# Kernel optimization log

Measured on AMD Instinct MI355X. Metric: run time of the kernel, lower is better.

## Reference

```python
import jax, jax.numpy as jnp
import numpy as np

N_NODES = 50000
N_EDGES = 800000
IN_SIZE, HID_SIZE, OUT_SIZE = 512, 128, 64


def _graph_conv(feat, src, dst, W, b, out_norm, in_norm, activation=None):
    # DGL GraphConv with norm='both': h' = D_in^{-1/2} A D_out^{-1/2} (X W) + b
    x = feat * out_norm[:, None]          # scale by source (out-degree) norm
    x = x @ W                             # dense transform first (in >= out)
    msg = x[src]                          # gather per-edge messages [E, d]
    agg = jax.ops.segment_sum(msg, dst, num_segments=N_NODES)
    h = agg * in_norm[:, None] + b
    if activation is not None:
        h = activation(h)
    return h


def setup_inputs() -> dict:
    key = jax.random.key(0)
    k1, k2, k3, k4, k5, k6, k7 = jax.random.split(key, 7)
    features = jax.random.normal(k1, (N_NODES, IN_SIZE), dtype=jnp.float32)
    src = jax.random.randint(k2, (N_EDGES,), 0, N_NODES, dtype=jnp.int64)
    dst = jax.random.randint(k3, (N_EDGES,), 0, N_NODES, dtype=jnp.int64)
    # Glorot-style init as in dglnn.GraphConv
    W1 = jax.random.normal(k4, (IN_SIZE, HID_SIZE), dtype=jnp.float32) * (1.0 / np.sqrt(IN_SIZE))
    b1 = jnp.zeros((HID_SIZE,), dtype=jnp.float32)
    W2 = jax.random.normal(k5, (HID_SIZE, OUT_SIZE), dtype=jnp.float32) * (1.0 / np.sqrt(HID_SIZE))
    b2 = jnp.zeros((OUT_SIZE,), dtype=jnp.float32)
    return {"features": features, "W1": W1, "b1": b1, "W2": W2, "b2": b2,
            "src": src, "dst": dst}


def reference(features, W1, b1, W2, b2, src, dst):
    ones = jnp.ones((N_EDGES,), dtype=features.dtype)
    out_deg = jax.ops.segment_sum(ones, src, num_segments=N_NODES)
    in_deg = jax.ops.segment_sum(ones, dst, num_segments=N_NODES)
    out_norm = jax.lax.rsqrt(jnp.clip(out_deg, 1.0))  # deg clamped to >=1 as in DGL
    in_norm = jax.lax.rsqrt(jnp.clip(in_deg, 1.0))
    h = _graph_conv(features, src, dst, W1, b1, out_norm, in_norm, activation=jax.nn.relu)
    # dropout omitted (eval mode)
    h = _graph_conv(h, src, dst, W2, b2, out_norm, in_norm, activation=None)
    return h
```

## Files before the change

### kernel.cpp

```cpp
#include <hip/hip_runtime.h>

#define N_NODES 50000
#define IN_SIZE 512
#define HID 128
#define OUT 64
#define NB 256
#define SHIFT 7
#define NBUCK 391
#define NBINS8 12500

typedef _Float16 f16x8 __attribute__((ext_vector_type(8)));
typedef _Float16 f16x4 __attribute__((ext_vector_type(4)));
typedef float    f32x4 __attribute__((ext_vector_type(4)));

__device__ __forceinline__ bool detect_w(const int* p, int t, int* sh) {
    if (t < 64) {
        unsigned long long m = __ballot(p[2 * t + 1] == 0);
        if (t == 0) *sh = (m == ~0ull) ? 1 : 0;
    }
    __syncthreads();
    return *sh != 0;
}

__device__ __forceinline__ int load_idx(const void* p, int e, bool w) {
    return w ? (int)((const long long*)p)[e] : ((const int*)p)[e];
}

__global__ __launch_bounds__(256) void k_hist_wt(const void* __restrict__ srcp,
                                                 const void* __restrict__ dstp,
                                                 int* __restrict__ hist,
                                                 unsigned int* __restrict__ spart,
                                                 int E, int EPB,
                                                 const float* __restrict__ W1, _Float16* __restrict__ W1T,
                                                 const float* __restrict__ W2, _Float16* __restrict__ W2T) {
    const int t = threadIdx.x, b = blockIdx.x;
    if (b >= NB) {
        int i = (b - NB) * 256 + t;
        if (i < IN_SIZE * HID) {
            int k = i >> 7, n = i & (HID - 1);
            W1T[(size_t)n * IN_SIZE + k] = (_Float16)W1[i];
        } else {
            int j = i - IN_SIZE * HID;
            if (j < HID * OUT) {
                int k = j >> 6, n = j & (OUT - 1);
                W2T[(size_t)n * HID + k] = (_Float16)W2[j];
            }
        }
        return;
    }
    __shared__ unsigned int sbins[NBINS8];
    __shared__ int dbins[NBUCK];
    __shared__ int shw;
    for (int i = t; i < NBINS8; i += 256) sbins[i] = 0;
    for (int i = t; i < NBUCK; i += 256) dbins[i] = 0;
    bool w = detect_w((const int*)dstp, t, &shw);
    __syncthreads();
    int eend = min(E, (b + 1) * EPB);
    for (int e = b * EPB + t; e < eend; e += 256) {
        int s = load_idx(srcp, e, w);
        int d = load_idx(dstp, e, w);
        atomicAdd(&dbins[d >> SHIFT], 1);
        atomicAdd(&sbins[s >> 2], 1u << ((s & 3) << 3));
    }
    __syncthreads();
    for (int i = t; i < NBUCK; i += 256) hist[i * NB + b] = dbins[i];
    for (int i = t; i < NBINS8; i += 256) spart[(size_t)b * NBINS8 + i] = sbins[i];
}

__global__ __launch_bounds__(256) void k_scanA(int* __restrict__ hist, int* __restrict__ bsum) {
    __shared__ int s[256];
    const int t = threadIdx.x, g = blockIdx.x;
    int v = hist[g * NB + t];
    s[t] = v;
    __syncthreads();
    for (int off = 1; off < 256; off <<= 1) {
        int u = (t >= off) ? s[t - off] : 0;
        __syncthreads();
        s[t] += u;
        __syncthreads();
    }
    hist[g * NB + t] = s[t] - v;
    if (t == 255) bsum[g] = s[255];
}

__global__ __launch_bounds__(512) void k_scanB(const int* __restrict__ bsum, int* __restrict__ bb) {
    __shared__ int s[512];
    const int t = threadIdx.x;
    int v = (t < NBUCK) ? bsum[t] : 0;
    s[t] = v;
    __syncthreads();
    for (int off = 1; off < 512; off <<= 1) {
        int u = (t >= off) ? s[t - off] : 0;
        __syncthreads();
        s[t] += u;
        __syncthreads();
    }
    if (t <= NBUCK) bb[t] = s[t] - v;
}

__global__ __launch_bounds__(256) void k_cscatter(const void* __restrict__ srcp,
                                                  const void* __restrict__ dstp,
                                                  const int* __restrict__ hist,
                                                  const int* __restrict__ bb,
                                                  unsigned int* __restrict__ tmp,
                                                  int E, int EPB) {
    __shared__ int cur[NBUCK];
    __shared__ int shw;
    const int t = threadIdx.x, b = blockIdx.x;
    for (int i = t; i < NBUCK; i += 256) cur[i] = hist[i * NB + b] + bb[i];
    bool w = detect_w((const int*)dstp, t, &shw);
    __syncthreads();
    int eend = min(E, (b + 1) * EPB);
    for (int e = b * EPB + t; e < eend; e += 256) {
        int s = load_idx(srcp, e, w);
        int d = load_idx(dstp, e, w);
        int pos = atomicAdd(&cur[d >> SHIFT], 1);
        tmp[pos] = (unsigned int)s | ((unsigned int)(d & 127) << 16);
    }
}

__global__ __launch_bounds__(256) void k_fine(const unsigned int* __restrict__ tmp,
                                              const int* __restrict__ bb,
                                              const unsigned int* __restrict__ partial,
                                              int* __restrict__ rp,
                                              int* __restrict__ esrc,
                                              float* __restrict__ innorm,
                                              float* __restrict__ onorm) {
    __shared__ int fcnt[128];
    __shared__ int sc[128];
    __shared__ int fcur[128];
    __shared__ int rs[256][4];
    const int t = threadIdx.x, u = blockIdx.x;
    const int e0 = bb[u], e1 = bb[u + 1];
    if (t < 128) fcnt[t] = 0;
    __syncthreads();
    for (int e = e0 + t; e < e1; e += 256)
        atomicAdd(&fcnt[tmp[e] >> 16], 1);
    {
        const int wrd = t & 31, grp = t >> 5;
        const int wd = u * 32 + wrd;
        int c0 = 0, c1 = 0, c2 = 0, c3 = 0;
        if (wd < NBINS8) {
            for (int b = grp * 32; b < grp * 32 + 32; ++b) {
                unsigned int v = partial[(size_t)b * NBINS8 + wd];
                c0 += (int)(v & 255u);
                c1 += (int)((v >> 8) & 255u);
                c2 += (int)((v >> 16) & 255u);
                c3 += (int)(v >> 24);
            }
        }
        rs[t][0] = c0; rs[t][1] = c1; rs[t][2] = c2; rs[t][3] = c3;
    }
    __syncthreads();
    if (t < 32) {
        const int wd = u * 32 + t;
        if (wd < NBINS8) {
            int d0 = 0, d1 = 0, d2 = 0, d3 = 0;
            for (int g = 0; g < 8; ++g) {
                d0 += rs[g * 32 + t][0]; d1 += rs[g * 32 + t][1];
                d2 += rs[g * 32 + t][2]; d3 += rs[g * 32 + t][3];
            }
            if (d0 < 1) d0 = 1; if (d1 < 1) d1 = 1;
            if (d2 < 1) d2 = 1; if (d3 < 1) d3 = 1;
            int n0 = 4 * wd;
            if (n0     < N_NODES) onorm[n0]     = 1.0f / sqrtf((float)d0);
            if (n0 + 1 < N_NODES) onorm[n0 + 1] = 1.0f / sqrtf((float)d1);
            if (n0 + 2 < N_NODES) onorm[n0 + 2] = 1.0f / sqrtf((float)d2);
            if (n0 + 3 < N_NODES) onorm[n0 + 3] = 1.0f / sqrtf((float)d3);
        }
    }
    if (t < 128) sc[t] = fcnt[t];
    __syncthreads();
    for (int off = 1; off < 128; off <<= 1) {
        int v = (t < 128 && t >= off) ? sc[t - off] : 0;
        __syncthreads();
        if (t < 128) sc[t] += v;
        __syncthreads();
    }
    if (t < 128) {
        int base = e0 + sc[t] - fcnt[t];
        fcur[t] = base;
        int node = u * 128 + t;
        if (node < N_NODES) {
            rp[node] = base;
            int c = fcnt[t]; if (c < 1) c = 1;
            innorm[node] = 1.0f / sqrtf((float)c);
        }
    }
    if (u == NBUCK - 1 && t == 0) rp[N_NODES] = e1;
    __syncthreads();
    for (int e = e0 + t; e < e1; e += 256) {
        unsigned int p = tmp[e];
        int pos = atomicAdd(&fcur[p >> 16], 1);
        esrc[pos] = (int)(p & 0xFFFFu);
    }
}

#define LDA 40
__global__ __launch_bounds__(256) void k_gemm1_mfma(const float* __restrict__ A,
                                                    const _Float16* __restrict__ BT,
                                                    const float* __restrict__ onorm,
                                                    _Float16* __restrict__ X) {
    __shared__ _Float16 As[64 * LDA];
    __shared__ _Float16 Bs[128 * LDA];
    const int tid  = threadIdx.x;
    const int wave = tid >> 6, lane = tid & 63;
    const int lm = lane & 15, lq = lane >> 4;
    const int row0 = blockIdx.x * 64;

    const int ar = tid >> 2, aq = tid & 3;
    int arow = row0 + ar; if (arow >= N_NODES) arow = N_NODES - 1;
    const float* aptr = A + (size_t)arow * IN_SIZE + aq * 8;
    _Float16* asd = &As[ar * LDA + aq * 8];
    const int bn = tid >> 1, bh = tid & 1;
    const _Float16* bptr = BT + (size_t)bn * IN_SIZE + bh * 16;
    _Float16* bsd = &Bs[bn * LDA + bh * 16];

    f32x4 acc[8];
#pragma unroll
    for (int nt = 0; nt < 8; ++nt) acc[nt] = (f32x4){0.f, 0.f, 0.f, 0.f};

    for (int k0 = 0; k0 < IN_SIZE; k0 += 32) {
        float4 a0 = *(const float4*)(aptr + k0);
        float4 a1 = *(const float4*)(aptr + k0 + 4);
        f16x8  b0 = *(const f16x8*)(bptr + k0);
        f16x8  b1 = *(const f16x8*)(bptr + k0 + 8);
        f16x8 ap = {(_Float16)a0.x, (_Float16)a0.y, (_Float16)a0.z, (_Float16)a0.w,
                    (_Float16)a1.x, (_Float16)a1.y, (_Float16)a1.z, (_Float16)a1.w};
        __syncthreads();
        *(f16x8*)asd       = ap;
        *(f16x8*)bsd       = b0;
        *(f16x8*)(bsd + 8) = b1;
        __syncthreads();
        f16x8 af = *(const f16x8*)&As[(wave * 16 + lm) * LDA + lq * 8];
#pragma unroll
        for (int nt = 0; nt < 8; ++nt) {
            f16x8 bf = *(const f16x8*)&Bs[(nt * 16 + lm) * LDA + lq * 8];
            acc[nt] = __builtin_amdgcn_mfma_f32_16x16x32_f16(af, bf, acc[nt], 0, 0, 0);
        }
    }
#pragma unroll
    for (int i = 0; i < 4; ++i) {
        int row = row0 + wave * 16 + lq * 4 + i;
        if (row < N_NODES) {
            float on = onorm[row];
            _Float16* o = X + (size_t)row * HID + lm;
#pragma unroll
            for (int nt = 0; nt < 8; ++nt)
                o[nt * 16] = (_Float16)(acc[nt][i] * on);
        }
    }
}

#define LDH 136
__global__ __launch_bounds__(256) void k_agg1_fused(const _Float16* __restrict__ X, const int* __restrict__ rp,
                                                    const int* __restrict__ esrc, const float* __restrict__ innorm,
                                                    const float* __restrict__ onorm, const float* __restrict__ b1,
                                                    const _Float16* __restrict__ W2T, _Float16* __restrict__ X2) {
    __shared__ _Float16 Hs[16 * LDH];
    const int t = threadIdx.x;
    const int ln = t >> 4;
    const int c  = (t & 15) << 3;
    const int n  = blockIdx.x * 16 + ln;
    const int e0 = rp[n], e1 = rp[n + 1];
    float a[8] = {0.f, 0.f, 0.f, 0.f, 0.f, 0.f, 0.f, 0.f};
    int e = e0;
    for (; e + 3 < e1; e += 4) {
        int s0 = esrc[e], s1 = esrc[e + 1], s2 = esrc[e + 2], s3 = esrc[e + 3];
        f16x8 v0 = *(const f16x8*)&X[(size_t)s0 * HID + c];
        f16x8 v1 = *(const f16x8*)&X[(size_t)s1 * HID + c];
        f16x8 v2 = *(const f16x8*)&X[(size_t)s2 * HID + c];
        f16x8 v3 = *(const f16x8*)&X[(size_t)s3 * HID + c];
#pragma unroll
        for (int j = 0; j < 8; ++j)
            a[j] += ((float)v0[j] + (float)v1[j]) + ((float)v2[j] + (float)v3[j]);
    }
    for (; e < e1; ++e) {
        f16x8 v = *(const f16x8*)&X[(size_t)esrc[e] * HID + c];
#pragma unroll
        for (int j = 0; j < 8; ++j) a[j] += (float)v[j];
    }
    const float inn = innorm[n], on = onorm[n];
    float4 bA = *(const float4*)&b1[c];
    float4 bB = *(const float4*)&b1[c + 4];
    const float bv[8] = {bA.x, bA.y, bA.z, bA.w, bB.x, bB.y, bB.z, bB.w};
    f16x8 h;
#pragma unroll
    for (int j = 0; j < 8; ++j)
        h[j] = (_Float16)(fmaxf(a[j] * inn + bv[j], 0.f) * on);
    *(f16x8*)&Hs[ln * LDH + c] = h;
    __syncthreads();

    const int wave = t >> 6, lane = t & 63;
    const int lm = lane & 15, lq = lane >> 4;
    f32x4 acc = (f32x4){0.f, 0.f, 0.f, 0.f};
#pragma unroll
    for (int k0 = 0; k0 < HID; k0 += 32) {
        f16x8 af = *(const f16x8*)&Hs[lm * LDH + k0 + lq * 8];
        f16x8 bf = *(const f16x8*)&W2T[(size_t)(wave * 16 + lm) * HID + k0 + lq * 8];
        acc = __builtin_amdgcn_mfma_f32_16x16x32_f16(af, bf, acc, 0, 0, 0);
    }
    const int n0 = blockIdx.x * 16;
#pragma unroll
    for (int i = 0; i < 4; ++i) {
        int row = n0 + lq * 4 + i;
        X2[(size_t)row * OUT + wave * 16 + lm] = (_Float16)acc[i];
    }
}

__global__ __launch_bounds__(256) void k_agg2(const _Float16* __restrict__ X2, const int* __restrict__ rp,
                                              const int* __restrict__ esrc, const float* __restrict__ innorm,
                                              const float* __restrict__ b2, float* __restrict__ out) {
    const int n = blockIdx.x * 32 + (threadIdx.x >> 3);
    const int c = (threadIdx.x & 7) << 3;
    if (n >= N_NODES) return;
    const int e0 = rp[n], e1 = rp[n + 1];
    float a[8] = {0.f, 0.f, 0.f, 0.f, 0.f, 0.f, 0.f, 0.f};
    int e = e0;
    for (; e + 3 < e1; e += 4) {
        int s0 = esrc[e], s1 = esrc[e + 1], s2 = esrc[e + 2], s3 = esrc[e + 3];
        f16x8 v0 = *(const f16x8*)&X2[(size_t)s0 * OUT + c];
        f16x8 v1 = *(const f16x8*)&X2[(size_t)s1 * OUT + c];
        f16x8 v2 = *(const f16x8*)&X2[(size_t)s2 * OUT + c];
        f16x8 v3 = *(const f16x8*)&X2[(size_t)s3 * OUT + c];
#pragma unroll
        for (int j = 0; j < 8; ++j)
            a[j] += ((float)v0[j] + (float)v1[j]) + ((float)v2[j] + (float)v3[j]);
    }
    for (; e < e1; ++e) {
        f16x8 v = *(const f16x8*)&X2[(size_t)esrc[e] * OUT + c];
#pragma unroll
        for (int j = 0; j < 8; ++j) a[j] += (float)v[j];
    }
    const float inn = innorm[n];
    float4 bA = *(const float4*)&b2[c];
    float4 bB = *(const float4*)&b2[c + 4];
    float* o = out + (size_t)n * OUT + c;
    *(float4*)o       = make_float4(a[0] * inn + bA.x, a[1] * inn + bA.y,
                                    a[2] * inn + bA.z, a[3] * inn + bA.w);
    *(float4*)(o + 4) = make_float4(a[4] * inn + bB.x, a[5] * inn + bB.y,
                                    a[6] * inn + bB.z, a[7] * inn + bB.w);
}

extern "C" void kernel_launch(void* const* d_in, const int* in_sizes, int n_in,
                              void* d_out, int out_size, void* d_ws, size_t ws_size,
                              hipStream_t stream) {
    const float* feat = (const float*)d_in[0];
    const float* W1   = (const float*)d_in[1];
    const float* b1   = (const float*)d_in[2];
    const float* W2   = (const float*)d_in[3];
    const float* b2   = (const float*)d_in[4];
    const void*  srcp = (const void*)d_in[5];
    const void*  dstp = (const void*)d_in[6];
    const int    E    = in_sizes[5];
    float* out = (float*)d_out;

    char* w = (char*)d_ws;
    size_t off = 0;
    auto alloc = [&](size_t bytes) -> void* {
        off = (off + 255) & ~(size_t)255;
        void* p = w + off;
        off += bytes;
        return p;
    };
    int*   hist    = (int*)alloc((size_t)NBUCK * NB * 4);
    int*   bsum    = (int*)alloc((size_t)NBUCK * 4);
    int*   bb      = (int*)alloc((size_t)(NBUCK + 1) * 4);
    int*   rp      = (int*)alloc((size_t)(N_NODES + 1) * 4);
    unsigned int* spart = (unsigned int*)alloc((size_t)NB * NBINS8 * 4);
    unsigned int* tmp   = (unsigned int*)alloc((size_t)E * 4);
    int*   esrc    = (int*)alloc((size_t)E * 4);
    float* onorm   = (float*)alloc((size_t)N_NODES * 4);
    float* innorm  = (float*)alloc((size_t)N_NODES * 4);
    _Float16* W1T  = (_Float16*)alloc((size_t)IN_SIZE * HID * 2);
    _Float16* W2T  = (_Float16*)alloc((size_t)HID * OUT * 2);
    _Float16* X1   = (_Float16*)alloc((size_t)N_NODES * HID * 2);
    _Float16* X2   = (_Float16*)alloc((size_t)N_NODES * OUT * 2);
    (void)ws_size; (void)n_in; (void)out_size;

    const int EPB = (E + NB - 1) / NB;
    const int WTB = (IN_SIZE * HID + HID * OUT + 255) / 256;

    k_hist_wt<<<NB + WTB, 256, 0, stream>>>(srcp, dstp, hist, spart, E, EPB, W1, W1T, W2, W2T);
    k_scanA<<<NBUCK, 256, 0, stream>>>(hist, bsum);
    k_scanB<<<1, 512, 0, stream>>>(bsum, bb);
    k_cscatter<<<NB, 256, 0, stream>>>(srcp, dstp, hist, bb, tmp, E, EPB);
    k_fine<<<NBUCK, 256, 0, stream>>>(tmp, bb, spart, rp, esrc, innorm, onorm);

    k_gemm1_mfma<<<(N_NODES + 63) / 64, 256, 0, stream>>>(feat, W1T, onorm, X1);
    k_agg1_fused<<<(N_NODES + 15) / 16, 256, 0, stream>>>(X1, rp, esrc, innorm, onorm, b1, W2T, X2);
    k_agg2<<<(N_NODES + 31) / 32, 256, 0, stream>>>(X2, rp, esrc, innorm, b2, out);
}
```

Baseline: 275.9 us.

## Double-buffer LDS tiles in first-layer MFMA GEMM and pad row stride

The first-layer feature GEMM now keeps two shared-memory tile buffers. Each step prefetches the next K-slice of A and B from global memory into registers while MFMAs run on the current slice, then writes it to the other buffer. This cuts the two barriers per K-step to one and hides global load latency behind compute. The LDS row stride also changes from 40 to 44 halves to alter the bank-conflict pattern. The cost is more LDS and registers per block, and 16-byte vector LDS accesses are no longer 16-byte aligned.

```diff
diff --git a/kernel.cpp b/kernel.cpp
--- a/kernel.cpp
+++ b/kernel.cpp
@@ -196,13 +196,13 @@
     }
 }
 
-#define LDA 40
+#define LDA 44
 __global__ __launch_bounds__(256) void k_gemm1_mfma(const float* __restrict__ A,
                                                     const _Float16* __restrict__ BT,
                                                     const float* __restrict__ onorm,
                                                     _Float16* __restrict__ X) {
-    __shared__ _Float16 As[64 * LDA];
-    __shared__ _Float16 Bs[128 * LDA];
+    __shared__ _Float16 As[2][64 * LDA];
+    __shared__ _Float16 Bs[2][128 * LDA];
     const int tid  = threadIdx.x;
     const int wave = tid >> 6, lane = tid & 63;
     const int lm = lane & 15, lq = lane >> 4;
@@ -211,32 +211,51 @@
     const int ar = tid >> 2, aq = tid & 3;
     int arow = row0 + ar; if (arow >= N_NODES) arow = N_NODES - 1;
     const float* aptr = A + (size_t)arow * IN_SIZE + aq * 8;
-    _Float16* asd = &As[ar * LDA + aq * 8];
     const int bn = tid >> 1, bh = tid & 1;
     const _Float16* bptr = BT + (size_t)bn * IN_SIZE + bh * 16;
-    _Float16* bsd = &Bs[bn * LDA + bh * 16];
 
     f32x4 acc[8];
 #pragma unroll
     for (int nt = 0; nt < 8; ++nt) acc[nt] = (f32x4){0.f, 0.f, 0.f, 0.f};
 
-    for (int k0 = 0; k0 < IN_SIZE; k0 += 32) {
-        float4 a0 = *(const float4*)(aptr + k0);
-        float4 a1 = *(const float4*)(aptr + k0 + 4);
-        f16x8  b0 = *(const f16x8*)(bptr + k0);
-        f16x8  b1 = *(const f16x8*)(bptr + k0 + 8);
+    {
+        float4 a0 = *(const float4*)(aptr);
+        float4 a1 = *(const float4*)(aptr + 4);
+        f16x8  b0 = *(const f16x8*)(bptr);
+        f16x8  b1 = *(const f16x8*)(bptr + 8);
         f16x8 ap = {(_Float16)a0.x, (_Float16)a0.y, (_Float16)a0.z, (_Float16)a0.w,
                     (_Float16)a1.x, (_Float16)a1.y, (_Float16)a1.z, (_Float16)a1.w};
-        __syncthreads();
-        *(f16x8*)asd       = ap;
-        *(f16x8*)bsd       = b0;
-        *(f16x8*)(bsd + 8) = b1;
-        __syncthreads();
-        f16x8 af = *(const f16x8*)&As[(wave * 16 + lm) * LDA + lq * 8];
+        *(f16x8*)&As[0][ar * LDA + aq * 8]      = ap;
+        *(f16x8*)&Bs[0][bn * LDA + bh * 16]     = b0;
+        *(f16x8*)&Bs[0][bn * LDA + bh * 16 + 8] = b1;
+    }
+    __syncthreads();
+
+#pragma unroll
+    for (int kt = 0; kt < IN_SIZE / 32; ++kt) {
+        const int k0 = kt * 32;
+        const int cur = kt & 1;
+        float4 na0, na1; f16x8 nb0, nb1;
+        const bool more = (k0 + 32) < IN_SIZE;
+        if (more) {
+            na0 = *(const float4*)(aptr + k0 + 32);
+            na1 = *(const float4*)(aptr + k0 + 36);
+            nb0 = *(const f16x8*)(bptr + k0 + 32);
+            nb1 = *(const f16x8*)(bptr + k0 + 40);
+        }
+        f16x8 af = *(const f16x8*)&As[cur][(wave * 16 + lm) * LDA + lq * 8];
 #pragma unroll
         for (int nt = 0; nt < 8; ++nt) {
-            f16x8 bf = *(const f16x8*)&Bs[(nt * 16 + lm) * LDA + lq * 8];
+            f16x8 bf = *(const f16x8*)&Bs[cur][(nt * 16 + lm) * LDA + lq * 8];
             acc[nt] = __builtin_amdgcn_mfma_f32_16x16x32_f16(af, bf, acc[nt], 0, 0, 0);
+        }
+        if (more) {
+            f16x8 ap = {(_Float16)na0.x, (_Float16)na0.y, (_Float16)na0.z, (_Float16)na0.w,
+                        (_Float16)na1.x, (_Float16)na1.y, (_Float16)na1.z, (_Float16)na1.w};
+            *(f16x8*)&As[cur ^ 1][ar * LDA + aq * 8]      = ap;
+            *(f16x8*)&Bs[cur ^ 1][bn * LDA + bh * 16]     = nb0;
+            *(f16x8*)&Bs[cur ^ 1][bn * LDA + bh * 16 + 8] = nb1;
+            __syncthreads();
         }
     }
 #pragma unroll
```

Result: no change. 271.7 us (-1.5%).
